# Optimization experiments

Measured on AMD Instinct MI355X. Metric: run time of the kernel, lower is better.

The kernel has to match this reference:

```python
import jax, jax.numpy as jnp
import numpy as np

N, C, HR, WR, HS, WS, S = 4, 128, 64, 64, 64, 64, 64


def setup_inputs() -> dict:
    key = jax.random.key(0)
    k1, k2, k3 = jax.random.split(key, 3)
    feat_ref = jax.random.normal(k1, (N, C, HR, WR), dtype=jnp.float32)
    feat_src = jax.random.normal(k2, (N, C, HS, WS), dtype=jnp.float32)
    # sampling locations in unnormalized source-pixel coordinates [0, WS)
    grids = jax.random.uniform(k3, (N, S, 2, HR, WR), dtype=jnp.float32) * WS
    mask = jnp.ones((N, S, HR, WR), dtype=jnp.float32)
    return {"feat_ref": feat_ref, "feat_src": feat_src, "grids": grids, "mask": mask}


def _corr_forward(feat_ref, feat_src, grids, mask):
    n, c, hr, wr = feat_ref.shape
    hs, ws = feat_src.shape[-2:]
    s = grids.shape[1]
    p = hr * wr
    fr = feat_ref.reshape(n, c, p)          # [N,C,P]
    fs = feat_src.reshape(n, c, hs * ws)    # [N,C,HsWs]
    # full pairwise correlation volume (normalize=False path)
    corr = jnp.einsum('ncp,ncq->npq', fr, fs)  # [N,P,HsWs]

    # grids NS2HrWr -> [N,P,2,S]  (matches permute(0,3,4,2,1).reshape)
    g = jnp.transpose(grids, (0, 3, 4, 2, 1)).reshape(n, p, 2, s)
    gx, gy = g[:, :, 0, :], g[:, :, 1, :]   # [N,P,S]

    # torch grid_sample, align_corners=False: normalized->pixel maps to coord-0.5
    ix = gx - 0.5
    iy = gy - 0.5
    x0 = jnp.floor(ix)
    y0 = jnp.floor(iy)
    wx1 = ix - x0
    wy1 = iy - y0
    x0i = x0.astype(jnp.int32)
    y0i = y0.astype(jnp.int32)

    out = jnp.zeros((n, p, s), corr.dtype)
    msum = jnp.zeros((n, p, s), corr.dtype)  # grid_sample of all-ones (zeros padding)
    for dx, wx in ((0, 1.0 - wx1), (1, wx1)):
        for dy, wy in ((0, 1.0 - wy1), (1, wy1)):
            xi = x0i + dx
            yi = y0i + dy
            inb = ((xi >= 0) & (xi < ws) & (yi >= 0) & (yi < hs)).astype(corr.dtype)
            idx = jnp.clip(yi, 0, hs - 1) * ws + jnp.clip(xi, 0, ws - 1)  # [N,P,S]
            val = jnp.take_along_axis(corr, idx, axis=-1)
            w = wx * wy * inb
            out = out + w * val
            msum = msum + w

    # mask[mask < 0.9999] = 0; mask[mask > 0] = 1
    corr_mask = jnp.where(msum < 0.9999, 0.0, 1.0).astype(corr.dtype)
    out = out * corr_mask

    # [N,P,S] -> [N,S,Hr,Wr]
    out = out.reshape(n, hr, wr, s).transpose(0, 3, 1, 2)
    corr_mask = corr_mask.reshape(n, hr, wr, s).transpose(0, 3, 1, 2)

    out = out * mask
    corr_mask = corr_mask * mask
    return out, corr_mask


def reference(feat_ref, feat_src, grids, mask):
    return _corr_forward(feat_ref, feat_src, grids, mask)
```

## Files before the change

kernel.cpp:

```cpp
#include <hip/hip_runtime.h>
#include <hip/hip_fp16.h>
#include <cstdint>
#include <cstddef>

#define NB 4
#define C 128
#define P 4096
#define S 64
#define Q 4096
#define WS_DIM 64
#define HS_DIM 64

#define PADR  80
#define NROWS 4256

__device__ __forceinline__ void gload_lds16(const void* g, void* l) {
  __builtin_amdgcn_global_load_lds(
      (const __attribute__((address_space(1))) unsigned int*)g,
      (__attribute__((address_space(3))) unsigned int*)l, 16, 0, 0);
}

__global__ __launch_bounds__(256) void transpose_fs_h(
    const float* __restrict__ fs, __half* __restrict__ ws) {
  __shared__ float tile[32][65];
  int b = blockIdx.x;
  int n  = b >> 8;
  int t  = b & 255;
  int rti = t & 3;
  int cti = t >> 2;
  int r0 = rti << 5, c0 = cti << 6;
  const float* Sp = fs + (size_t)n * C * P;
  __half*      Dp = ws + (size_t)n * NROWS * C + (size_t)PADR * C;
  int tx = threadIdx.x & 15, ty = threadIdx.x >> 4;
#pragma unroll
  for (int i = 0; i < 2; ++i) {
    int row = ty + 16 * i;
    float4 v = *reinterpret_cast<const float4*>(
        &Sp[(size_t)(r0 + row) * P + c0 + tx * 4]);
    tile[row][tx * 4 + 0] = v.x;
    tile[row][tx * 4 + 1] = v.y;
    tile[row][tx * 4 + 2] = v.z;
    tile[row][tx * 4 + 3] = v.w;
  }
  __syncthreads();
  int ox = threadIdx.x & 7, oy = threadIdx.x >> 3;
#pragma unroll
  for (int i = 0; i < 2; ++i) {
    int prow = oy + 32 * i;
    __half2 h01 = __floats2half2_rn(tile[ox * 4 + 0][prow], tile[ox * 4 + 1][prow]);
    __half2 h23 = __floats2half2_rn(tile[ox * 4 + 2][prow], tile[ox * 4 + 3][prow]);
    uint2 pk;
    pk.x = *reinterpret_cast<unsigned int*>(&h01);
    pk.y = *reinterpret_cast<unsigned int*>(&h23);
    *reinterpret_cast<uint2*>(&Dp[(size_t)(c0 + prow) * C + r0 + ox * 4]) = pk;
  }
}

__global__ __launch_bounds__(256) void corr_main(
    const __half* __restrict__ ws, const float* __restrict__ fr_g,
    const float* __restrict__ grids, const float* __restrict__ mask,
    float* __restrict__ out, float* __restrict__ cmo) {
  __shared__ __align__(16) unsigned char stg[4][16384];
  __shared__ int    s_qb[4][68];
  __shared__ float4 s_w[4][65];
  __shared__ float  s_cmm[4][68];
  __shared__ float  s_out[4][68];
  __shared__ float  fr_lds[4][132];

  int b    = blockIdx.x;
  int xcd  = b & 7;
  int n    = xcd >> 1;
  int half = xcd & 1;
  int grp  = b >> 3;
  int wv   = threadIdx.x >> 6;
  int lane = threadIdx.x & 63;
  int t    = threadIdx.x;
  int p_base = ((half << 9) + grp) << 2;

#pragma unroll
  for (int i = 0; i < 2; ++i) {
    int e  = t + 256 * i;
    int c  = e >> 2;
    int po = e & 3;
    fr_lds[po][c] = fr_g[((size_t)n * C + c) * P + p_base + po];
  }

  {
    int s  = t >> 2;
    int po = t & 3;
    int pp = p_base + po;
    float gx = grids[(((size_t)n * S + s) * 2 + 0) * P + pp];
    float gy = grids[(((size_t)n * S + s) * 2 + 1) * P + pp];
    float mval = mask[((size_t)n * S + s) * P + pp];
    float ix = gx - 0.5f, iy = gy - 0.5f;
    float x0f = floorf(ix), y0f = floorf(iy);
    float wx1 = ix - x0f, wy1 = iy - y0f;
    float wx0 = 1.0f - wx1, wy0 = 1.0f - wy1;
    int x0 = (int)x0f, y0 = (int)y0f;
    bool bx0 = (x0 >= 0) & (x0 < WS_DIM);
    bool bx1 = (x0 >= -1) & (x0 < WS_DIM - 1);
    bool by0 = (y0 >= 0) & (y0 < HS_DIM);
    bool by1 = (y0 >= -1) & (y0 < HS_DIM - 1);
    float w00 = (bx0 & by0) ? wx0 * wy0 : 0.0f;
    float w01 = (bx0 & by1) ? wx0 * wy1 : 0.0f;
    float w10 = (bx1 & by0) ? wx1 * wy0 : 0.0f;
    float w11 = (bx1 & by1) ? wx1 * wy1 : 0.0f;
    float msum = ((w00 + w01) + w10) + w11;
    float cm  = (msum < 0.9999f) ? 0.0f : 1.0f;
    float cmm = cm * mval;
    int qb = y0 * WS_DIM + x0;
    qb = max(-PADR, min(qb, 4110));
    s_qb[po][s]  = qb;
    s_w[po][s]   = make_float4(w00, w10, w01, w11);
    s_cmm[po][s] = cmm;
    cmo[((size_t)n * S + s) * P + pp] = cmm;
  }
  __syncthreads();

  int o  = lane & 7;
  int sl = lane >> 3;
  float fr0[8], fr1[8];
  {
    float4 a = *reinterpret_cast<const float4*>(&fr_lds[wv][o * 8]);
    float4 bq = *reinterpret_cast<const float4*>(&fr_lds[wv][o * 8 + 4]);
    fr0[0] = a.x; fr0[1] = a.y; fr0[2] = a.z; fr0[3] = a.w;
    fr0[4] = bq.x; fr0[5] = bq.y; fr0[6] = bq.z; fr0[7] = bq.w;
    float4 c = *reinterpret_cast<const float4*>(&fr_lds[wv][64 + o * 8]);
    float4 d = *reinterpret_cast<const float4*>(&fr_lds[wv][64 + o * 8 + 4]);
    fr1[0] = c.x; fr1[1] = c.y; fr1[2] = c.z; fr1[3] = c.w;
    fr1[4] = d.x; fr1[5] = d.y; fr1[6] = d.z; fr1[7] = d.w;
  }
  const __half* fsn = ws + (size_t)n * NROWS * C + (size_t)PADR * C;
  unsigned char* mystg = &stg[wv][0];

#pragma unroll 1
  for (int r = 0; r < 4; ++r) {
    __builtin_amdgcn_sched_barrier(0);
#pragma unroll
    for (int h = 0; h < 2; ++h) {
      int s = r * 16 + h * 8 + sl;
      int qb = s_qb[wv][s];
#pragma unroll
      for (int y = 0; y < 2; ++y) {
        const __half* src = fsn + (long)(qb + y * 64) * C + o * 8;
#pragma unroll
        for (int j = 0; j < 4; ++j)
          gload_lds16(src + j * 64, mystg + ((h * 2 + y) * 4 + j) * 1024);
      }
    }

#pragma unroll
    for (int h = 0; h < 2; ++h) {
      if (h == 0) { asm volatile("s_waitcnt vmcnt(8)" ::: "memory"); }
      else        { asm volatile("s_waitcnt vmcnt(0)" ::: "memory"); }
      int s = r * 16 + h * 8 + sl;
      float4 w4  = s_w[wv][s];
      float  cms = s_cmm[wv][s];
      float acc = 0.0f;
#pragma unroll
      for (int y = 0; y < 2; ++y) {
        const unsigned char* base = mystg + ((h * 2 + y) * 4) * 1024 + lane * 16;
        const __half2* b0 = reinterpret_cast<const __half2*>(base);
        const __half2* b1 = reinterpret_cast<const __half2*>(base + 1024);
        const __half2* b2 = reinterpret_cast<const __half2*>(base + 2048);
        const __half2* b3 = reinterpret_cast<const __half2*>(base + 3072);
        float d0 = 0.0f, d1 = 0.0f;
#pragma unroll
        for (int i = 0; i < 4; ++i) {
          float2 f0 = __half22float2(b0[i]);
          float2 f1 = __half22float2(b1[i]);
          float2 f2 = __half22float2(b2[i]);
          float2 f3 = __half22float2(b3[i]);
          d0 = fmaf(fr0[2 * i], f0.x, d0);
          d0 = fmaf(fr0[2 * i + 1], f0.y, d0);
          d0 = fmaf(fr1[2 * i], f1.x, d0);
          d0 = fmaf(fr1[2 * i + 1], f1.y, d0);
          d1 = fmaf(fr0[2 * i], f2.x, d1);
          d1 = fmaf(fr0[2 * i + 1], f2.y, d1);
          d1 = fmaf(fr1[2 * i], f3.x, d1);
          d1 = fmaf(fr1[2 * i + 1], f3.y, d1);
        }
        float wA = (y == 0) ? w4.x : w4.z;
        float wB = (y == 0) ? w4.y : w4.w;
        acc = fmaf(wA, d0, acc);
        acc = fmaf(wB, d1, acc);
      }
      acc += __shfl_xor(acc, 1);
      acc += __shfl_xor(acc, 2);
      acc += __shfl_xor(acc, 4);
      if (o == 0) s_out[wv][s] = acc * cms;
    }
  }
  __syncthreads();
  {
    int s = t >> 2, w2 = t & 3;
    out[((size_t)n * S + s) * P + (p_base + w2)] = s_out[w2][s];
  }
}

extern "C" void kernel_launch(void* const* d_in, const int* in_sizes, int n_in,
                              void* d_out, int out_size, void* d_ws, size_t ws_size,
                              hipStream_t stream) {
  const float* feat_ref = (const float*)d_in[0];
  const float* feat_src = (const float*)d_in[1];
  const float* grids    = (const float*)d_in[2];
  const float* mask     = (const float*)d_in[3];
  __half* ws = (__half*)d_ws;
  float* out = (float*)d_out;
  float* cmo = out + (size_t)NB * S * P;

  transpose_fs_h<<<1024, 256, 0, stream>>>(feat_src, ws);
  corr_main<<<4096, 256, 0, stream>>>(ws, feat_ref, grids, mask, out, cmo);
}
```

Measured before the change: 140.4 us.

## Compute full correlation volume with MFMA GEMM then gather bilinear samples

Replaces the per-sample gathered dot products with a dense fp16 MFMA GEMM that materializes the full N×P×Q correlation volume in fp16 workspace, followed by a light gather kernel that does bilinear interpolation from it. The intent is to trade redundant 4×64 dot products per pixel for tensor-core throughput. In exchange it writes and reads a 128 MB padded correlation buffer and adds an extra launch, and it also rounds the correlation values to fp16.

```diff
diff --git a/kernel.cpp b/kernel.cpp
--- a/kernel.cpp
+++ b/kernel.cpp
@@ -11,191 +11,152 @@
 #define WS_DIM 64
 #define HS_DIM 64
 
-#define PADR  80
-#define NROWS 4256
+#define QPAD0 72
+#define QROW  4240
+#define ROWH  136
 
-__device__ __forceinline__ void gload_lds16(const void* g, void* l) {
-  __builtin_amdgcn_global_load_lds(
-      (const __attribute__((address_space(1))) unsigned int*)g,
-      (__attribute__((address_space(3))) unsigned int*)l, 16, 0, 0);
+using half8 = __attribute__((ext_vector_type(8))) _Float16;
+using f32x4 = __attribute__((ext_vector_type(4))) float;
+
+
+__global__ __launch_bounds__(256) void convert_h(
+    const float* __restrict__ fr, const float* __restrict__ fs,
+    __half* __restrict__ ws) {
+  int b = blockIdx.x;
+  const float* src = (b < 2048) ? fr : fs;
+  __half* dst = ws + ((b < 2048) ? 0 : (size_t)NB * C * P);
+  size_t i = (((size_t)(b & 2047)) * 256 + threadIdx.x) * 4;
+  float4 v = *reinterpret_cast<const float4*>(src + i);
+  __half2 lo = __floats2half2_rn(v.x, v.y);
+  __half2 hi = __floats2half2_rn(v.z, v.w);
+  uint2 pk;
+  pk.x = *reinterpret_cast<unsigned int*>(&lo);
+  pk.y = *reinterpret_cast<unsigned int*>(&hi);
+  *reinterpret_cast<uint2*>(dst + i) = pk;
 }
 
-__global__ __launch_bounds__(256) void transpose_fs_h(
-    const float* __restrict__ fs, __half* __restrict__ ws) {
-  __shared__ float tile[32][65];
+__global__ __launch_bounds__(256) void gemm_corr(
+    const __half* __restrict__ ws, __half* __restrict__ corr) {
+  const __half* fr_h = ws;
+  const __half* fs_h = ws + (size_t)NB * C * P;
+  __shared__ __half A_lds[C][ROWH];
+  __shared__ __half B_lds[C][ROWH];
+
   int b = blockIdx.x;
-  int n  = b >> 8;
-  int t  = b & 255;
-  int rti = t & 3;
-  int cti = t >> 2;
-  int r0 = rti << 5, c0 = cti << 6;
-  const float* Sp = fs + (size_t)n * C * P;
-  __half*      Dp = ws + (size_t)n * NROWS * C + (size_t)PADR * C;
-  int tx = threadIdx.x & 15, ty = threadIdx.x >> 4;
+  int xcd = b & 7;
+  int n = xcd >> 1;
+  int g = ((xcd & 1) << 9) + (b >> 3);
+  int p0 = (g >> 5) << 7;
+  int q0 = (g & 31) << 7;
+  int t = threadIdx.x;
+
+  {
+    int k = t >> 1, h = t & 1;
+    const uint4* sA = reinterpret_cast<const uint4*>(
+        fr_h + ((size_t)n * C + k) * P + p0 + h * 64);
+    const uint4* sB = reinterpret_cast<const uint4*>(
+        fs_h + ((size_t)n * C + k) * Q + q0 + h * 64);
+    uint4* dA = reinterpret_cast<uint4*>(&A_lds[k][h * 64]);
+    uint4* dB = reinterpret_cast<uint4*>(&B_lds[k][h * 64]);
 #pragma unroll
-  for (int i = 0; i < 2; ++i) {
-    int row = ty + 16 * i;
-    float4 v = *reinterpret_cast<const float4*>(
-        &Sp[(size_t)(r0 + row) * P + c0 + tx * 4]);
-    tile[row][tx * 4 + 0] = v.x;
-    tile[row][tx * 4 + 1] = v.y;
-    tile[row][tx * 4 + 2] = v.z;
-    tile[row][tx * 4 + 3] = v.w;
+    for (int j = 0; j < 8; ++j) dA[j] = sA[j];
+#pragma unroll
+    for (int j = 0; j < 8; ++j) dB[j] = sB[j];
   }
   __syncthreads();
-  int ox = threadIdx.x & 7, oy = threadIdx.x >> 3;
+
+  int wv = t >> 6, lane = t & 63;
+  int wm = (wv >> 1) * 64, wn = (wv & 1) * 64;
+  int lm = lane & 15, kg = (lane >> 4) * 8;
+  f32x4 acc[4][4] = {};
+
 #pragma unroll
-  for (int i = 0; i < 2; ++i) {
-    int prow = oy + 32 * i;
-    __half2 h01 = __floats2half2_rn(tile[ox * 4 + 0][prow], tile[ox * 4 + 1][prow]);
-    __half2 h23 = __floats2half2_rn(tile[ox * 4 + 2][prow], tile[ox * 4 + 3][prow]);
-    uint2 pk;
-    pk.x = *reinterpret_cast<unsigned int*>(&h01);
-    pk.y = *reinterpret_cast<unsigned int*>(&h23);
-    *reinterpret_cast<uint2*>(&Dp[(size_t)(c0 + prow) * C + r0 + ox * 4]) = pk;
+  for (int ks = 0; ks < 4; ++ks) {
+    int kb = ks * 32 + kg;
+    half8 af[4], bf[4];
+#pragma unroll
+    for (int f = 0; f < 4; ++f) {
+#pragma unroll
+      for (int i = 0; i < 8; ++i) {
+        af[f][i] = *reinterpret_cast<const _Float16*>(&A_lds[kb + i][wm + f * 16 + lm]);
+        bf[f][i] = *reinterpret_cast<const _Float16*>(&B_lds[kb + i][wn + f * 16 + lm]);
+      }
+    }
+#pragma unroll
+    for (int mf = 0; mf < 4; ++mf)
+#pragma unroll
+      for (int nf = 0; nf < 4; ++nf)
+        acc[mf][nf] = __builtin_amdgcn_mfma_f32_16x16x32_f16(
+            af[mf], bf[nf], acc[mf][nf], 0, 0, 0);
+  }
+  __syncthreads();
+
+  int r0 = (lane >> 4) * 4;
+#pragma unroll
+  for (int mf = 0; mf < 4; ++mf)
+#pragma unroll
+    for (int nf = 0; nf < 4; ++nf)
+#pragma unroll
+      for (int r = 0; r < 4; ++r)
+        A_lds[wm + mf * 16 + r0 + r][wn + nf * 16 + lm] =
+            __float2half(acc[mf][nf][r]);
+  __syncthreads();
+  {
+    int row = t >> 1, h = t & 1;
+    const uint4* sL = reinterpret_cast<const uint4*>(&A_lds[row][h * 64]);
+    uint4* dG = reinterpret_cast<uint4*>(
+        corr + ((size_t)(n * P + p0 + row)) * QROW + QPAD0 + q0 + h * 64);
+#pragma unroll
+    for (int j = 0; j < 8; ++j) dG[j] = sL[j];
   }
 }
 
-__global__ __launch_bounds__(256) void corr_main(
-    const __half* __restrict__ ws, const float* __restrict__ fr_g,
+__global__ __launch_bounds__(256) void gather_corr(
+    const __half* __restrict__ corr,
     const float* __restrict__ grids, const float* __restrict__ mask,
     float* __restrict__ out, float* __restrict__ cmo) {
-  __shared__ __align__(16) unsigned char stg[4][16384];
-  __shared__ int    s_qb[4][68];
-  __shared__ float4 s_w[4][65];
-  __shared__ float  s_cmm[4][68];
-  __shared__ float  s_out[4][68];
-  __shared__ float  fr_lds[4][132];
+  int b = blockIdx.x;
+  int xcd = b & 7;
+  int n = xcd >> 1;
+  int half = xcd & 1;
+  int grp = b >> 3;
+  int p_base = ((half << 9) + grp) << 2;
+  int t = threadIdx.x;
+  int s = t >> 2, po = t & 3;
+  int p = p_base + po;
 
-  int b    = blockIdx.x;
-  int xcd  = b & 7;
-  int n    = xcd >> 1;
-  int half = xcd & 1;
-  int grp  = b >> 3;
-  int wv   = threadIdx.x >> 6;
-  int lane = threadIdx.x & 63;
-  int t    = threadIdx.x;
-  int p_base = ((half << 9) + grp) << 2;
+  float gx = grids[(((size_t)n * S + s) * 2 + 0) * P + p];
+  float gy = grids[(((size_t)n * S + s) * 2 + 1) * P + p];
+  float mval = mask[((size_t)n * S + s) * P + p];
+  float ix = gx - 0.5f, iy = gy - 0.5f;
+  float x0f = floorf(ix), y0f = floorf(iy);
+  float wx1 = ix - x0f, wy1 = iy - y0f;
+  float wx0 = 1.0f - wx1, wy0 = 1.0f - wy1;
+  int x0 = (int)x0f, y0 = (int)y0f;
+  bool bx0 = (x0 >= 0) & (x0 < WS_DIM);
+  bool bx1 = (x0 >= -1) & (x0 < WS_DIM - 1);
+  bool by0 = (y0 >= 0) & (y0 < HS_DIM);
+  bool by1 = (y0 >= -1) & (y0 < HS_DIM - 1);
+  float w00 = (bx0 & by0) ? wx0 * wy0 : 0.0f;
+  float w01 = (bx0 & by1) ? wx0 * wy1 : 0.0f;
+  float w10 = (bx1 & by0) ? wx1 * wy0 : 0.0f;
+  float w11 = (bx1 & by1) ? wx1 * wy1 : 0.0f;
+  float msum = ((w00 + w01) + w10) + w11;
+  float cm = (msum < 0.9999f) ? 0.0f : 1.0f;
+  float cmm = cm * mval;
 
-#pragma unroll
-  for (int i = 0; i < 2; ++i) {
-    int e  = t + 256 * i;
-    int c  = e >> 2;
-    int po = e & 3;
-    fr_lds[po][c] = fr_g[((size_t)n * C + c) * P + p_base + po];
-  }
+  int qb = y0 * WS_DIM + x0;
+  qb = max(-QPAD0, min(qb, 4102));
+  const __half* row = corr + ((size_t)(n * P + p)) * QROW + QPAD0 + qb;
+  float v00 = __half2float(row[0]);
+  float v10 = __half2float(row[1]);
+  float v01 = __half2float(row[64]);
+  float v11 = __half2float(row[65]);
+  float val = fmaf(w11, v11, fmaf(w10, v10, fmaf(w01, v01, w00 * v00)));
 
-  {
-    int s  = t >> 2;
-    int po = t & 3;
-    int pp = p_base + po;
-    float gx = grids[(((size_t)n * S + s) * 2 + 0) * P + pp];
-    float gy = grids[(((size_t)n * S + s) * 2 + 1) * P + pp];
-    float mval = mask[((size_t)n * S + s) * P + pp];
-    float ix = gx - 0.5f, iy = gy - 0.5f;
-    float x0f = floorf(ix), y0f = floorf(iy);
-    float wx1 = ix - x0f, wy1 = iy - y0f;
-    float wx0 = 1.0f - wx1, wy0 = 1.0f - wy1;
-    int x0 = (int)x0f, y0 = (int)y0f;
-    bool bx0 = (x0 >= 0) & (x0 < WS_DIM);
-    bool bx1 = (x0 >= -1) & (x0 < WS_DIM - 1);
-    bool by0 = (y0 >= 0) & (y0 < HS_DIM);
-    bool by1 = (y0 >= -1) & (y0 < HS_DIM - 1);
-    float w00 = (bx0 & by0) ? wx0 * wy0 : 0.0f;
-    float w01 = (bx0 & by1) ? wx0 * wy1 : 0.0f;
-    float w10 = (bx1 & by0) ? wx1 * wy0 : 0.0f;
-    float w11 = (bx1 & by1) ? wx1 * wy1 : 0.0f;
-    float msum = ((w00 + w01) + w10) + w11;
-    float cm  = (msum < 0.9999f) ? 0.0f : 1.0f;
-    float cmm = cm * mval;
-    int qb = y0 * WS_DIM + x0;
-    qb = max(-PADR, min(qb, 4110));
-    s_qb[po][s]  = qb;
-    s_w[po][s]   = make_float4(w00, w10, w01, w11);
-    s_cmm[po][s] = cmm;
-    cmo[((size_t)n * S + s) * P + pp] = cmm;
-  }
-  __syncthreads();
-
-  int o  = lane & 7;
-  int sl = lane >> 3;
-  float fr0[8], fr1[8];
-  {
-    float4 a = *reinterpret_cast<const float4*>(&fr_lds[wv][o * 8]);
-    float4 bq = *reinterpret_cast<const float4*>(&fr_lds[wv][o * 8 + 4]);
-    fr0[0] = a.x; fr0[1] = a.y; fr0[2] = a.z; fr0[3] = a.w;
-    fr0[4] = bq.x; fr0[5] = bq.y; fr0[6] = bq.z; fr0[7] = bq.w;
-    float4 c = *reinterpret_cast<const float4*>(&fr_lds[wv][64 + o * 8]);
-    float4 d = *reinterpret_cast<const float4*>(&fr_lds[wv][64 + o * 8 + 4]);
-    fr1[0] = c.x; fr1[1] = c.y; fr1[2] = c.z; fr1[3] = c.w;
-    fr1[4] = d.x; fr1[5] = d.y; fr1[6] = d.z; fr1[7] = d.w;
-  }
-  const __half* fsn = ws + (size_t)n * NROWS * C + (size_t)PADR * C;
-  unsigned char* mystg = &stg[wv][0];
-
-#pragma unroll 1
-  for (int r = 0; r < 4; ++r) {
-    __builtin_amdgcn_sched_barrier(0);
-#pragma unroll
-    for (int h = 0; h < 2; ++h) {
-      int s = r * 16 + h * 8 + sl;
-      int qb = s_qb[wv][s];
-#pragma unroll
-      for (int y = 0; y < 2; ++y) {
-        const __half* src = fsn + (long)(qb + y * 64) * C + o * 8;
-#pragma unroll
-        for (int j = 0; j < 4; ++j)
-          gload_lds16(src + j * 64, mystg + ((h * 2 + y) * 4 + j) * 1024);
-      }
-    }
-
-#pragma unroll
-    for (int h = 0; h < 2; ++h) {
-      if (h == 0) { asm volatile("s_waitcnt vmcnt(8)" ::: "memory"); }
-      else        { asm volatile("s_waitcnt vmcnt(0)" ::: "memory"); }
-      int s = r * 16 + h * 8 + sl;
-      float4 w4  = s_w[wv][s];
-      float  cms = s_cmm[wv][s];
-      float acc = 0.0f;
-#pragma unroll
-      for (int y = 0; y < 2; ++y) {
-        const unsigned char* base = mystg + ((h * 2 + y) * 4) * 1024 + lane * 16;
-        const __half2* b0 = reinterpret_cast<const __half2*>(base);
-        const __half2* b1 = reinterpret_cast<const __half2*>(base + 1024);
-        const __half2* b2 = reinterpret_cast<const __half2*>(base + 2048);
-        const __half2* b3 = reinterpret_cast<const __half2*>(base + 3072);
-        float d0 = 0.0f, d1 = 0.0f;
-#pragma unroll
-        for (int i = 0; i < 4; ++i) {
-          float2 f0 = __half22float2(b0[i]);
-          float2 f1 = __half22float2(b1[i]);
-          float2 f2 = __half22float2(b2[i]);
-          float2 f3 = __half22float2(b3[i]);
-          d0 = fmaf(fr0[2 * i], f0.x, d0);
-          d0 = fmaf(fr0[2 * i + 1], f0.y, d0);
-          d0 = fmaf(fr1[2 * i], f1.x, d0);
-          d0 = fmaf(fr1[2 * i + 1], f1.y, d0);
-          d1 = fmaf(fr0[2 * i], f2.x, d1);
-          d1 = fmaf(fr0[2 * i + 1], f2.y, d1);
-          d1 = fmaf(fr1[2 * i], f3.x, d1);
-          d1 = fmaf(fr1[2 * i + 1], f3.y, d1);
-        }
-        float wA = (y == 0) ? w4.x : w4.z;
-        float wB = (y == 0) ? w4.y : w4.w;
-        acc = fmaf(wA, d0, acc);
-        acc = fmaf(wB, d1, acc);
-      }
-      acc += __shfl_xor(acc, 1);
-      acc += __shfl_xor(acc, 2);
-      acc += __shfl_xor(acc, 4);
-      if (o == 0) s_out[wv][s] = acc * cms;
-    }
-  }
-  __syncthreads();
-  {
-    int s = t >> 2, w2 = t & 3;
-    out[((size_t)n * S + s) * P + (p_base + w2)] = s_out[w2][s];
-  }
+  size_t oi = ((size_t)n * S + s) * P + p;
+  out[oi] = val * cmm;
+  cmo[oi] = cmm;
 }
 
 extern "C" void kernel_launch(void* const* d_in, const int* in_sizes, int n_in,
@@ -205,10 +166,12 @@
   const float* feat_src = (const float*)d_in[1];
   const float* grids    = (const float*)d_in[2];
   const float* mask     = (const float*)d_in[3];
-  __half* ws = (__half*)d_ws;
+  __half* ws   = (__half*)d_ws;
+  __half* corr = (__half*)((char*)d_ws + (size_t)(16u << 20));
   float* out = (float*)d_out;
   float* cmo = out + (size_t)NB * S * P;
 
-  transpose_fs_h<<<1024, 256, 0, stream>>>(feat_src, ws);
-  corr_main<<<4096, 256, 0, stream>>>(ws, feat_ref, grids, mask, out, cmo);
+  convert_h<<<4096, 256, 0, stream>>>(feat_ref, feat_src, ws);
+  gemm_corr<<<4096, 256, 0, stream>>>(ws, corr);
+  gather_corr<<<4096, 256, 0, stream>>>(corr, grids, mask, out, cmo);
 }
```

New measurement: 174.9 us. 1.25x slower.
